# Kernel optimization log

Hardware: AMD Instinct MI355X
Metric: run time of the kernel (lower is better)

Reference implementation:

```python
import jax, jax.numpy as jnp
import numpy as np

DIM = 1024
CTX_DIM = 768

def setup_inputs() -> dict:
    key = jax.random.key(0)
    ks = jax.random.split(key, 12)
    B, Sq, Skv = 8, 2048, 2048
    s_d = 1.0 / np.sqrt(DIM)
    s_c = 1.0 / np.sqrt(CTX_DIM)
    return {
        "x": jax.random.normal(ks[0], (B, Sq, DIM), jnp.float32),
        "context": jax.random.normal(ks[1], (B, Skv, CTX_DIM), jnp.float32),
        # nn.Linear weights are [out_features, in_features]
        "Wq": jax.random.uniform(ks[2], (DIM, DIM), jnp.float32, -s_d, s_d),
        "bq": jax.random.uniform(ks[3], (DIM,), jnp.float32, -s_d, s_d),
        "Wk": jax.random.uniform(ks[4], (DIM, CTX_DIM), jnp.float32, -s_c, s_c),
        "bk": jax.random.uniform(ks[5], (DIM,), jnp.float32, -s_c, s_c),
        "Wv": jax.random.uniform(ks[6], (DIM, CTX_DIM), jnp.float32, -s_c, s_c),
        "bv": jax.random.uniform(ks[7], (DIM,), jnp.float32, -s_c, s_c),
        "Wo": jax.random.uniform(ks[8], (DIM, DIM), jnp.float32, -s_d, s_d),
        "bo": jax.random.uniform(ks[9], (DIM,), jnp.float32, -s_d, s_d),
    }

def reference(x, context, Wq, bq, Wk, bk, Wv, bv, Wo, bo):
    # q: [B,Sq,D], k,v: [B,Skv,D]
    q = jnp.einsum('bsi,di->bsd', x, Wq) + bq
    k = jnp.einsum('bsc,dc->bsd', context, Wk) + bk
    v = jnp.einsum('bsc,dc->bsd', context, Wv) + bv
    scale = 1.0 / jnp.sqrt(jnp.asarray(q.shape[-1], q.dtype))
    scores = jnp.einsum('bqd,bkd->bqk', q, k) * scale  # [B,Sq,Skv]
    att = jax.nn.softmax(scores, axis=-1)
    out = jnp.einsum('bqk,bkd->bqd', att, v)
    return jnp.einsum('bqd,od->bqo', out, Wo) + bo
```

## Files before the change

### kernel.cpp

```cpp
#include <hip/hip_runtime.h>

typedef unsigned short u16;
typedef unsigned int   u32;
typedef __attribute__((ext_vector_type(8))) short short8;
typedef __attribute__((ext_vector_type(4))) float f32x4;

#define DIM   1024
#define CDIM  768
#define BATCH 8
#define SQ    2048
#define SKV   2048

__device__ __forceinline__ u16 f2bf(float f) {
    union { float f; u32 u; } c; c.f = f;
    u32 u = c.u;
    u += 0x7fffu + ((u >> 16) & 1u);
    return (u16)(u >> 16);
}

__device__ __forceinline__ void async_copy16(const u16* g, u16* l) {
    __builtin_amdgcn_global_load_lds(
        (const __attribute__((address_space(1))) void*)g,
        (__attribute__((address_space(3))) void*)l,
        16, 0, 0);
}

__device__ __forceinline__ void cvt4(const float* s, u16* d, int i) {
    float4 f = ((const float4*)s)[i];
    ushort4 o;
    o.x = f2bf(f.x); o.y = f2bf(f.y); o.z = f2bf(f.z); o.w = f2bf(f.w);
    ((ushort4*)d)[i] = o;
}

__global__ __launch_bounds__(256)
void conv_xc(const float* __restrict__ x, const float* __restrict__ ctx,
             u16* __restrict__ dx, u16* __restrict__ dc)
{
    int i = blockIdx.x * 256 + threadIdx.x;
    if (i < 4194304) cvt4(x, dx, i);
    else             cvt4(ctx, dc, i - 4194304);
}

__global__ __launch_bounds__(256)
void conv_w(const float* __restrict__ Wq, const float* __restrict__ Wk,
            const float* __restrict__ Wv, const float* __restrict__ Wo,
            u16* __restrict__ dq, u16* __restrict__ dk,
            u16* __restrict__ dv, u16* __restrict__ dw)
{
    int i = blockIdx.x * 256 + threadIdx.x;
    if      (i < 262144) cvt4(Wq, dq, i);
    else if (i < 458752) cvt4(Wk, dk, i - 262144);
    else if (i < 655360) cvt4(Wv, dv, i - 458752);
    else                 cvt4(Wo, dw, i - 655360);
}

__device__ __forceinline__ void stage_A(const u16* __restrict__ G, long ld, long k0,
                                        u16* lbase, int p, int w, int lane)
{
    const int srow = lane >> 3;
    const int sch  = (lane & 7) ^ srow;
#pragma unroll
    for (int q = 0; q < 2; ++q) {
        int rb = q * 128 + p * 64 + w * 8;
        async_copy16(G + (long)(rb + srow) * ld + k0 + sch * 8, lbase + rb * 64);
    }
}

__device__ __forceinline__ void stage_B(const u16* __restrict__ G, long ld, long k0,
                                        u16* lbase, int p, int w, int lane)
{
    const int srow = lane >> 3;
    const int sch  = (lane & 7) ^ srow;
#pragma unroll
    for (int q = 0; q < 2; ++q) {
        int rb = q * 128 + (w >> 2) * 64 + p * 32 + (w & 3) * 8;
        async_copy16(G + (long)(rb + srow) * ld + k0 + sch * 8, lbase + rb * 64);
    }
}


#define SB() __builtin_amdgcn_sched_barrier(0)
#define FENCE_BAR() do { SB(); __builtin_amdgcn_s_barrier(); SB(); } while (0)

#define LOAD_A(Xs, mh)                                                         \
    do {                                                                       \
        _Pragma("unroll") for (int kc = 0; kc < 2; ++kc)                       \
        _Pragma("unroll") for (int i = 0; i < 4; ++i) {                        \
            int R = wm * 128 + (mh) * 64 + i * 16 + l15;                       \
            a[kc][i] = *(const short8*)&(Xs)[R * 64 +                          \
                         (((kc * 4 + quad) ^ (l15 & 7)) * 8)];                 \
        }                                                                      \
    } while (0)

#define LOAD_B(Xs, nh, dst)                                                    \
    do {                                                                       \
        _Pragma("unroll") for (int kc = 0; kc < 2; ++kc)                       \
        _Pragma("unroll") for (int j = 0; j < 2; ++j) {                        \
            int R = wn * 64 + (nh) * 32 + j * 16 + l15;                        \
            dst[kc][j] = *(const short8*)&(Xs)[R * 64 +                        \
                         (((kc * 4 + quad) ^ (l15 & 7)) * 8)];                 \
        }                                                                      \
    } while (0)

#define MFMA_Q(mh, nh, bb)                                                     \
    do {                                                                       \
        _Pragma("unroll") for (int kc = 0; kc < 2; ++kc)                       \
        _Pragma("unroll") for (int i = 0; i < 4; ++i)                          \
        _Pragma("unroll") for (int j = 0; j < 2; ++j)                          \
            acc[(mh) * 4 + i][(nh) * 2 + j] =                                  \
                __builtin_amdgcn_mfma_f32_16x16x32_bf16(                       \
                    a[kc][i], bb[kc][j],                                       \
                    acc[(mh) * 4 + i][(nh) * 2 + j], 0, 0, 0);                 \
    } while (0)

#define TILE_ITER(CUR, TT)                                                     \
    do {                                                                       \
        u16* As = &smem[CUR][0][0];                                            \
        u16* Bs = &smem[CUR][1][0];                                            \
        u16* An = &smem[(CUR) ^ 1][0][0];                                      \
        const long kA = kcl((TT) + 1);                                         \
        const long kB = kcl((TT) + 2);                                         \
                                                \
        LOAD_A(As, 0);                                                         \
        LOAD_B(Bs, 0, b0);                                                     \
        stage_A(gA, lda, kA, An, 0, w, lane);                                  \
        FENCE_BAR();                                                           \
        asm volatile("s_waitcnt lgkmcnt(0)");                                  \
        SB();                                                                  \
        __builtin_amdgcn_s_setprio(1);                                         \
        MFMA_Q(0, 0, b0);                                                      \
        __builtin_amdgcn_s_setprio(0);                                         \
        FENCE_BAR();                                                           \
                                                \
        LOAD_B(Bs, 1, b1);                                                     \
        stage_A(gA, lda, kA, An, 1, w, lane);                                  \
        FENCE_BAR();                                                           \
        asm volatile("s_waitcnt lgkmcnt(0)");                                  \
        SB();                                                                  \
        __builtin_amdgcn_s_setprio(1);                                         \
        MFMA_Q(0, 1, b1);                                                      \
        __builtin_amdgcn_s_setprio(0);                                         \
        asm volatile("s_waitcnt vmcnt(8)");                                    \
        SB();                                                                  \
        FENCE_BAR();                                                           \
                                                \
        LOAD_A(As, 1);                                                         \
        stage_B(gB, ldb, kB, Bs, 0, w, lane);                                  \
        FENCE_BAR();                                                           \
        asm volatile("s_waitcnt lgkmcnt(0)");                                  \
        SB();                                                                  \
        __builtin_amdgcn_s_setprio(1);                                         \
        MFMA_Q(1, 0, b0);                                                      \
        __builtin_amdgcn_s_setprio(0);                                         \
        FENCE_BAR();                                                           \
                                                \
        stage_B(gB, ldb, kB, Bs, 1, w, lane);                                  \
        FENCE_BAR();                                                           \
        __builtin_amdgcn_s_setprio(1);                                         \
        MFMA_Q(1, 1, b1);                                                      \
        __builtin_amdgcn_s_setprio(0);                                         \
        asm volatile("s_waitcnt vmcnt(6)");                                    \
        SB();                                                                  \
        FENCE_BAR();                                                           \
    } while (0)

template<int BIAS_MODE, int OUT_MODE>
__global__ __launch_bounds__(512, 2)
void gemm_nt(const u16* __restrict__ A, int lda_, long sA,
             const u16* __restrict__ Bw, int ldb_, long sB,
             const float* __restrict__ bias,
             void* __restrict__ Cout, int ldc_, long sC,
             int K, float scale, float* __restrict__ lsum)
{
    __shared__ u16 smem[2][2][256 * 64];
    const int t    = threadIdx.x;
    const int lane = t & 63;
    const int w    = t >> 6;
    const int wm   = w >> 2;
    const int wn   = w & 3;
    const int l15  = lane & 15;
    const int quad = lane >> 4;
    const long lda = lda_, ldb = ldb_, ldc = ldc_;
    const long m0 = (long)blockIdx.x * 256;
    const long n0 = (long)blockIdx.y * 256;
    const u16* gA = A  + (long)blockIdx.z * sA + m0 * lda;
    const u16* gB = Bw + (long)blockIdx.z * sB + n0 * ldb;
    const int NT = K >> 6;
    const long kmax = (long)K - 64;
    auto kcl = [&](int tt) -> long { long k = (long)tt * 64; return k < kmax ? k : kmax; };

    short8 a[2][4], b0[2][2], b1[2][2];
    const f32x4 fz = {0.f, 0.f, 0.f, 0.f};
    f32x4 acc[8][4];
#pragma unroll
    for (int i = 0; i < 8; ++i)
#pragma unroll
        for (int j = 0; j < 4; ++j) acc[i][j] = fz;

    stage_A(gA, lda, 0, &smem[0][0][0], 0, w, lane);
    stage_A(gA, lda, 0, &smem[0][0][0], 1, w, lane);
    stage_B(gB, ldb, 0, &smem[0][1][0], 0, w, lane);
    stage_B(gB, ldb, 0, &smem[0][1][0], 1, w, lane);
    stage_B(gB, ldb, kcl(1), &smem[1][1][0], 0, w, lane);
    stage_B(gB, ldb, kcl(1), &smem[1][1][0], 1, w, lane);
    asm volatile("s_waitcnt vmcnt(4)");
    FENCE_BAR();

    for (int T = 0; T < NT; T += 2) {
        TILE_ITER(0, T);
        TILE_ITER(1, T + 1);
    }

    float invl[8][4];
    if (BIAS_MODE == 3) {
        const long lbase = (long)blockIdx.z * (long)gridDim.x * 256 + m0 + wm * 128;
#pragma unroll
        for (int mi = 0; mi < 8; ++mi)
#pragma unroll
            for (int r = 0; r < 4; ++r)
                invl[mi][r] = 1.f / lsum[lbase + mi * 16 + quad * 4 + r];
    }

    float rowpart[8][4];
    if (OUT_MODE == 2) {
#pragma unroll
        for (int mi = 0; mi < 8; ++mi)
#pragma unroll
            for (int r = 0; r < 4; ++r) rowpart[mi][r] = 0.f;
    }

#pragma unroll
    for (int mi = 0; mi < 8; ++mi) {
#pragma unroll
        for (int nj = 0; nj < 4; ++nj) {
            long n = n0 + wn * 64 + nj * 16 + l15;
#pragma unroll
            for (int r = 0; r < 4; ++r) {
                long m = m0 + wm * 128 + mi * 16 + quad * 4 + r;
                float v = acc[mi][nj][r];
                if (BIAS_MODE == 0) v += bias[n];
                else if (BIAS_MODE == 1) v += bias[m];
                v *= scale;
                if (OUT_MODE == 2) { v = __expf(v); rowpart[mi][r] += v; }
                if (BIAS_MODE == 3) v *= invl[mi][r];
                long off = (long)blockIdx.z * sC + m * ldc + n;
                if (OUT_MODE == 1) ((float*)Cout)[off] = v;
                else               ((u16*)Cout)[off]   = f2bf(v);
            }
        }
    }

    if (OUT_MODE == 2) {
#pragma unroll
        for (int mi = 0; mi < 8; ++mi)
#pragma unroll
            for (int r = 0; r < 4; ++r) {
                float p = rowpart[mi][r];
                p += __shfl_xor(p, 1);
                p += __shfl_xor(p, 2);
                p += __shfl_xor(p, 4);
                p += __shfl_xor(p, 8);
                if (l15 == 0)
                    atomicAdd(&lsum[(long)blockIdx.z * (long)gridDim.x * 256 +
                                    m0 + wm * 128 + mi * 16 + quad * 4 + r], p);
            }
    }
}

extern "C" void kernel_launch(void* const* d_in, const int* in_sizes, int n_in,
                              void* d_out, int out_size, void* d_ws, size_t ws_size,
                              hipStream_t stream)
{
    const float* x   = (const float*)d_in[0];
    const float* ctx = (const float*)d_in[1];
    const float* Wq  = (const float*)d_in[2];
    const float* bq  = (const float*)d_in[3];
    const float* Wk  = (const float*)d_in[4];
    const float* bk  = (const float*)d_in[5];
    const float* Wv  = (const float*)d_in[6];
    const float* bv  = (const float*)d_in[7];
    const float* Wo  = (const float*)d_in[8];
    const float* bo  = (const float*)d_in[9];

    const int MQ  = BATCH * SQ;
    const int NX  = MQ * DIM;
    const int NC  = MQ * CDIM;
    const int NWQ = DIM * DIM;
    const int NWK = DIM * CDIM;

    u16* ws     = (u16*)d_ws;
    u16* xo_bf  = ws;
    u16* ctx_bf = xo_bf + NX;
    u16* k_bf   = ctx_bf + NC;
    u16* vt_bf  = k_bf + NX;
    u16* wq_bf  = vt_bf + NX;
    u16* wk_bf  = wq_bf + NWQ;
    u16* wv_bf  = wk_bf + NWK;
    u16* wo_bf  = wv_bf + NWK;
    u16* S      = wo_bf + NWQ;
    float* lsum = (float*)(S + (long)MQ * SKV);
    u16* q_bf   = (u16*)d_out;

    hipMemsetAsync(lsum, 0, MQ * sizeof(float), stream);

    conv_xc<<<(NX + NC) / 1024, 256, 0, stream>>>(x, ctx, xo_bf, ctx_bf);
    conv_w<<<(2 * NWQ + 2 * NWK) / 1024, 256, 0, stream>>>(
        Wq, Wk, Wv, Wo, wq_bf, wk_bf, wv_bf, wo_bf);

    gemm_nt<0, 0><<<dim3(MQ / 256, DIM / 256, 1), 512, 0, stream>>>(
        xo_bf, DIM, 0, wq_bf, DIM, 0, bq, q_bf, DIM, 0, DIM, 0.03125f, nullptr);
    gemm_nt<0, 0><<<dim3(MQ / 256, DIM / 256, 1), 512, 0, stream>>>(
        ctx_bf, CDIM, 0, wk_bf, CDIM, 0, bk, k_bf, DIM, 0, CDIM, 1.0f, nullptr);
    gemm_nt<1, 0><<<dim3(DIM / 256, MQ / 256, 1), 512, 0, stream>>>(
        wv_bf, CDIM, 0, ctx_bf, CDIM, 0, bv, vt_bf, MQ, 0, CDIM, 1.0f, nullptr);

    gemm_nt<2, 2><<<dim3(SQ / 256, SKV / 256, BATCH), 512, 0, stream>>>(
        q_bf, DIM, (long)SQ * DIM, k_bf, DIM, (long)SKV * DIM,
        nullptr, S, SKV, (long)SQ * SKV, DIM, 1.0f, lsum);

    gemm_nt<3, 0><<<dim3(SQ / 256, DIM / 256, BATCH), 512, 0, stream>>>(
        S, SKV, (long)SQ * SKV, vt_bf, MQ, (long)SKV,
        nullptr, xo_bf, DIM, (long)SQ * DIM, SKV, 1.0f, lsum);

    gemm_nt<0, 1><<<dim3(MQ / 256, DIM / 256, 1), 512, 0, stream>>>(
        xo_bf, DIM, 0, wo_bf, DIM, 0, bo, d_out, DIM, 0, DIM, 1.0f, nullptr);
}
```

Before: 451.2 us.

## Use simple 128x128 single-buffered GEMM for attention score and PV stages

Adds a simpler 128x128-tile, 256-thread GEMM kernel with a single LDS buffer and a sync per k-step. The original 256x256 pipelined kernel is renamed and kept for the projections. The two batched attention GEMMs (QK^T with exp and row-sum, and PV with normalization) now launch the new kernel with more, smaller blocks. This loses the software pipelining and the larger reuse of the tuned kernel, in exchange for more blocks per launch and simpler scheduling.

```diff
diff --git a/kernel.cpp b/kernel.cpp
--- a/kernel.cpp
+++ b/kernel.cpp
@@ -54,6 +54,123 @@
     else                 cvt4(Wo, dw, i - 655360);
 }
 
+template<int BIAS_MODE, int OUT_MODE>
+__global__ __launch_bounds__(256, 2)
+void gemm_nt(const u16* __restrict__ A, int lda, long sA,
+             const u16* __restrict__ Bw, int ldb, long sB,
+             const float* __restrict__ bias,
+             void* __restrict__ Cout, int ldc, long sC,
+             int K, float scale, float* __restrict__ lsum)
+{
+    __shared__ u16 As[128 * 64];
+    __shared__ u16 Bs[128 * 64];
+    const int t    = threadIdx.x;
+    const int lane = t & 63;
+    const int w    = t >> 6;
+    const int l15  = lane & 15;
+    const int quad = lane >> 4;
+    const int wm = w >> 1, wn = w & 1;
+    const long m0 = (long)blockIdx.x * 128;
+    const long n0 = (long)blockIdx.y * 128;
+    A  += (long)blockIdx.z * sA;
+    Bw += (long)blockIdx.z * sB;
+
+    const int srow   = lane >> 3;
+    const int schunk = (lane & 7) ^ srow;
+
+    const f32x4 fz = {0.f, 0.f, 0.f, 0.f};
+    f32x4 acc[4][4];
+#pragma unroll
+    for (int i = 0; i < 4; ++i)
+#pragma unroll
+        for (int j = 0; j < 4; ++j) acc[i][j] = fz;
+
+    for (int k0 = 0; k0 < K; k0 += 64) {
+#pragma unroll
+        for (int j = 0; j < 4; ++j) {
+            int rb = w * 32 + j * 8;
+            async_copy16(A  + (m0 + rb + srow) * (long)lda + k0 + schunk * 8, &As[rb * 64]);
+            async_copy16(Bw + (n0 + rb + srow) * (long)ldb + k0 + schunk * 8, &Bs[rb * 64]);
+        }
+        __syncthreads();
+#pragma unroll
+        for (int kc = 0; kc < 2; ++kc) {
+            short8 a[4], b[4];
+#pragma unroll
+            for (int i = 0; i < 4; ++i) {
+                int R = wm * 64 + i * 16 + l15;
+                a[i] = *(const short8*)&As[R * 64 + (((kc * 4 + quad) ^ (l15 & 7)) * 8)];
+            }
+#pragma unroll
+            for (int j = 0; j < 4; ++j) {
+                int R = wn * 64 + j * 16 + l15;
+                b[j] = *(const short8*)&Bs[R * 64 + (((kc * 4 + quad) ^ (l15 & 7)) * 8)];
+            }
+#pragma unroll
+            for (int i = 0; i < 4; ++i)
+#pragma unroll
+                for (int j = 0; j < 4; ++j)
+                    acc[i][j] = __builtin_amdgcn_mfma_f32_16x16x32_bf16(a[i], b[j], acc[i][j], 0, 0, 0);
+        }
+        __syncthreads();
+    }
+
+    float invl[4][4];
+    if (BIAS_MODE == 3) {
+        const long lbase = (long)blockIdx.z * gridDim.x * 128 + m0 + wm * 64;
+#pragma unroll
+        for (int i = 0; i < 4; ++i)
+#pragma unroll
+            for (int r = 0; r < 4; ++r)
+                invl[i][r] = 1.f / lsum[lbase + i * 16 + quad * 4 + r];
+    }
+
+    float rowpart[4][4];
+    if (OUT_MODE == 2) {
+#pragma unroll
+        for (int i = 0; i < 4; ++i)
+#pragma unroll
+            for (int r = 0; r < 4; ++r) rowpart[i][r] = 0.f;
+    }
+
+#pragma unroll
+    for (int i = 0; i < 4; ++i) {
+#pragma unroll
+        for (int j = 0; j < 4; ++j) {
+            long n = n0 + wn * 64 + j * 16 + l15;
+#pragma unroll
+            for (int r = 0; r < 4; ++r) {
+                long m = m0 + wm * 64 + i * 16 + quad * 4 + r;
+                float v = acc[i][j][r];
+                if (BIAS_MODE == 0) v += bias[n];
+                else if (BIAS_MODE == 1) v += bias[m];
+                v *= scale;
+                if (OUT_MODE == 2) { v = __expf(v); rowpart[i][r] += v; }
+                if (BIAS_MODE == 3) v *= invl[i][r];
+                long off = (long)blockIdx.z * sC + m * (long)ldc + n;
+                if (OUT_MODE == 1) ((float*)Cout)[off] = v;
+                else               ((u16*)Cout)[off]   = f2bf(v);
+            }
+        }
+    }
+
+    if (OUT_MODE == 2) {
+#pragma unroll
+        for (int i = 0; i < 4; ++i)
+#pragma unroll
+            for (int r = 0; r < 4; ++r) {
+                float p = rowpart[i][r];
+                p += __shfl_xor(p, 1);
+                p += __shfl_xor(p, 2);
+                p += __shfl_xor(p, 4);
+                p += __shfl_xor(p, 8);
+                if (l15 == 0)
+                    atomicAdd(&lsum[(long)blockIdx.z * gridDim.x * 128 +
+                                    m0 + wm * 64 + i * 16 + quad * 4 + r], p);
+            }
+    }
+}
+
 __device__ __forceinline__ void stage_A(const u16* __restrict__ G, long ld, long k0,
                                         u16* lbase, int p, int w, int lane)
 {
@@ -77,7 +194,6 @@
         async_copy16(G + (long)(rb + srow) * ld + k0 + sch * 8, lbase + rb * 64);
     }
 }
-
 
 #define SB() __builtin_amdgcn_sched_barrier(0)
 #define FENCE_BAR() do { SB(); __builtin_amdgcn_s_barrier(); SB(); } while (0)
@@ -166,11 +282,11 @@
 
 template<int BIAS_MODE, int OUT_MODE>
 __global__ __launch_bounds__(512, 2)
-void gemm_nt(const u16* __restrict__ A, int lda_, long sA,
-             const u16* __restrict__ Bw, int ldb_, long sB,
-             const float* __restrict__ bias,
-             void* __restrict__ Cout, int ldc_, long sC,
-             int K, float scale, float* __restrict__ lsum)
+void gemm_nt8(const u16* __restrict__ A, int lda_, long sA,
+              const u16* __restrict__ Bw, int ldb_, long sB,
+              const float* __restrict__ bias,
+              void* __restrict__ Cout, int ldc_, long sC,
+              int K, float scale, float* __restrict__ lsum)
 {
     __shared__ u16 smem[2][2][256 * 64];
     const int t    = threadIdx.x;
@@ -307,21 +423,21 @@
     conv_w<<<(2 * NWQ + 2 * NWK) / 1024, 256, 0, stream>>>(
         Wq, Wk, Wv, Wo, wq_bf, wk_bf, wv_bf, wo_bf);
 
-    gemm_nt<0, 0><<<dim3(MQ / 256, DIM / 256, 1), 512, 0, stream>>>(
+    gemm_nt8<0, 0><<<dim3(MQ / 256, DIM / 256, 1), 512, 0, stream>>>(
         xo_bf, DIM, 0, wq_bf, DIM, 0, bq, q_bf, DIM, 0, DIM, 0.03125f, nullptr);
-    gemm_nt<0, 0><<<dim3(MQ / 256, DIM / 256, 1), 512, 0, stream>>>(
+    gemm_nt8<0, 0><<<dim3(MQ / 256, DIM / 256, 1), 512, 0, stream>>>(
         ctx_bf, CDIM, 0, wk_bf, CDIM, 0, bk, k_bf, DIM, 0, CDIM, 1.0f, nullptr);
-    gemm_nt<1, 0><<<dim3(DIM / 256, MQ / 256, 1), 512, 0, stream>>>(
+    gemm_nt8<1, 0><<<dim3(DIM / 256, MQ / 256, 1), 512, 0, stream>>>(
         wv_bf, CDIM, 0, ctx_bf, CDIM, 0, bv, vt_bf, MQ, 0, CDIM, 1.0f, nullptr);
 
-    gemm_nt<2, 2><<<dim3(SQ / 256, SKV / 256, BATCH), 512, 0, stream>>>(
+    gemm_nt<2, 2><<<dim3(SQ / 128, SKV / 128, BATCH), 256, 0, stream>>>(
         q_bf, DIM, (long)SQ * DIM, k_bf, DIM, (long)SKV * DIM,
         nullptr, S, SKV, (long)SQ * SKV, DIM, 1.0f, lsum);
 
-    gemm_nt<3, 0><<<dim3(SQ / 256, DIM / 256, BATCH), 512, 0, stream>>>(
+    gemm_nt<3, 0><<<dim3(SQ / 128, DIM / 128, BATCH), 256, 0, stream>>>(
         S, SKV, (long)SQ * SKV, vt_bf, MQ, (long)SKV,
         nullptr, xo_bf, DIM, (long)SQ * DIM, SKV, 1.0f, lsum);
 
-    gemm_nt<0, 1><<<dim3(MQ / 256, DIM / 256, 1), 512, 0, stream>>>(
+    gemm_nt8<0, 1><<<dim3(MQ / 256, DIM / 256, 1), 512, 0, stream>>>(
         xo_bf, DIM, 0, wo_bf, DIM, 0, bo, d_out, DIM, 0, DIM, 1.0f, nullptr);
 }
```

New measurement: 472.7 us. 4.8% more time.
